# Optimization experiments

Measured on AMD Instinct MI355X. Metric: run time of the kernel, lower is better.

Reference implementation:

```python
import jax, jax.numpy as jnp
import numpy as np
from jax import lax

B, C, H, W = 16, 256, 64, 64
KNUM, KS, STRIDE, PAD, RED, GROUPS = 4, 3, 1, 1, 16, 4
BN_EPS = 1e-5


def setup_inputs() -> dict:
    key = jax.random.key(0)
    ks = jax.random.split(key, 12)
    f = jax.random.normal
    half, red = C // 2, C // RED
    return {
        "x": f(ks[0], (B, C, H, W), jnp.float32),
        "att_conv1d_w": f(ks[1], (3,), jnp.float32) * 0.5,                      # shared Conv1d(1,1,3) in Attention
        "att_out_w": f(ks[2], (C, C), jnp.float32) * (2.0 / C) ** 0.5,          # out_channel_conv2d 1x1
        "att_kernel_w": f(ks[3], (KNUM, C), jnp.float32) * (2.0 / C) ** 0.5,    # kernel_conv2d 1x1
        "ede_weight": f(ks[4], (KNUM, C, C, KS, KS), jnp.float32) * (2.0 / (C * KS * KS)) ** 0.5,
        "lga_conv1d_w": f(ks[5], (3,), jnp.float32) * 0.5,                      # LGA Conv1d(1,1,3) with bias
        "lga_conv1d_b": f(ks[6], (1,), jnp.float32) * 0.1,
        "lga_mlp_w1": f(ks[7], (red, half), jnp.float32) * (2.0 / half) ** 0.5,  # mlp conv 1x1 (no bias)
        "lga_mlp_w2": f(ks[8], (half, red), jnp.float32) * (2.0 / red) ** 0.5,
        "bn_gamma": jnp.ones((C,), jnp.float32),
        "bn_beta": jnp.zeros((C,), jnp.float32),
    }


def _conv1d_same(v_bc, w3):
    # 1-channel cross-correlation along the channel axis, pad=1 (PyTorch Conv1d)
    y = lax.conv_general_dilated(v_bc[:, None, :], w3[None, None, :], (1,), [(1, 1)],
                                 dimension_numbers=("NCH", "OIH", "NCH"))
    return y[:, 0, :]


def reference(x, att_conv1d_w, att_out_w, att_kernel_w, ede_weight,
              lga_conv1d_w, lga_conv1d_b, lga_mlp_w1, lga_mlp_w2,
              bn_gamma, bn_beta):
    b, c, h, w = x.shape

    # ---- EDE (Q branch): dynamic per-sample conv ----
    gap = x.mean(axis=(2, 3))                              # (b, c) global avg pool
    t = _conv1d_same(gap, att_conv1d_w)                    # shared conv1d over channels
    in_att = jax.nn.sigmoid(t)[:, :, None, None]           # (b, c, 1, 1)
    out_att = jax.nn.sigmoid(t @ att_out_w.T)[:, :, None, None]
    k_att = jax.nn.softmax(t @ att_kernel_w.T, axis=1)     # (b, KNUM)
    agg_w = jnp.einsum("bk,koipq->boipq", k_att, ede_weight)  # (b, C, C, KS, KS)
    x_mod = x * in_att

    def per_sample(xi, wi):  # xi: (C,H,W), wi: (C,C,KS,KS)
        return lax.conv_general_dilated(xi[None], wi, (STRIDE, STRIDE),
                                        [(PAD, PAD), (PAD, PAD)])[0]

    Q = jax.vmap(per_sample)(x_mod, agg_w) * out_att       # (b, C, H, W)

    # ---- LGA (K branch) ----
    half = c // 2
    in1, in2 = x[:, :half], x[:, half:]
    s = _conv1d_same(in1.mean(axis=(2, 3)), lga_conv1d_w) + lga_conv1d_b
    x1 = in1 * jax.nn.sigmoid(s)[:, :, None, None]

    def mlp(v):  # (b, half) -> (b, half); 1x1 convs on (b,half,1,1) == matmuls
        return jax.nn.relu(v @ lga_mlp_w1.T) @ lga_mlp_w2.T

    ch = jax.nn.sigmoid(mlp(in2.max(axis=(2, 3))) + mlp(in2.mean(axis=(2, 3))))
    y2 = in2 * ch[:, :, None, None]
    K = jnp.concatenate([x1, y2], axis=1)
    # channel shuffle with GROUPS groups
    K = K.reshape(b, GROUPS, c // GROUPS, h, w).transpose(0, 2, 1, 3, 4).reshape(b, c, h, w)

    # ---- fuse + BatchNorm (training-mode batch stats) + ReLU ----
    z = Q + K
    mean = z.mean(axis=(0, 2, 3))
    var = z.var(axis=(0, 2, 3))
    zn = (z - mean[None, :, None, None]) * lax.rsqrt(var[None, :, None, None] + BN_EPS)
    return jax.nn.relu(zn * bn_gamma[None, :, None, None] + bn_beta[None, :, None, None])
```

## Files before the change

kernel.cpp:

```cpp
#include <hip/hip_runtime.h>
#include <hip/hip_bf16.h>
#include <stdint.h>

#define HW_ 4096

typedef float f32x4 __attribute__((ext_vector_type(4)));
typedef short bf16x8 __attribute__((ext_vector_type(8)));

__device__ __forceinline__ unsigned short f2bf(float f) {
  __hip_bfloat16 h = __float2bfloat16(f);
  return *reinterpret_cast<unsigned short*>(&h);
}
__device__ __forceinline__ float sigmoidf_(float x) { return 1.f / (1.f + __expf(-x)); }

__device__ __forceinline__ void glds16(const void* g, void* l) {
  __builtin_amdgcn_global_load_lds(
      (const __attribute__((address_space(1))) unsigned int*)g,
      (__attribute__((address_space(3))) unsigned int*)l, 16, 0, 0);
}

__global__ void k_pre(const float* __restrict__ x, unsigned short* __restrict__ xtr,
                      float* __restrict__ psum, float* __restrict__ pmax) {
  int hwb = blockIdx.x;
  int cb = blockIdx.y;
  int b = blockIdx.z;
  int t = threadIdx.x;
  __shared__ float sv[64][65];
  int h16 = t & 15, g = t >> 4;
#pragma unroll
  for (int i = 0; i < 4; ++i) {
    int c_l = g + i * 16;
    float4 v = *reinterpret_cast<const float4*>(
        x + (((size_t)b * 256 + cb * 64 + c_l) << 12) + hwb * 64 + h16 * 4);
    *reinterpret_cast<float4*>(&sv[c_l][h16 * 4]) = v;
  }
  __syncthreads();
  {
    int c_l = t >> 2, q = t & 3;
    float s16 = 0.f, m16 = -3.4e38f;
#pragma unroll
    for (int j = 0; j < 16; ++j) {
      float vv = sv[c_l][q * 16 + j];
      s16 += vv; m16 = fmaxf(m16, vv);
    }
    s16 += __shfl_xor(s16, 1); s16 += __shfl_xor(s16, 2);
    m16 = fmaxf(m16, __shfl_xor(m16, 1)); m16 = fmaxf(m16, __shfl_xor(m16, 2));
    if (q == 0) {
      int c = cb * 64 + c_l;
      psum[(((size_t)b * 256 + c) << 6) + hwb] = s16;
      pmax[(((size_t)b * 256 + c) << 6) + hwb] = m16;
    }
  }
#pragma unroll
  for (int i = 0; i < 2; ++i) {
    int fp = t + i * 256;
    int hw2 = fp >> 3;
    int cp = (fp & 7) * 8;
    uint4 uu;
    uu.x = (unsigned)f2bf(sv[cp + 0][hw2]) | ((unsigned)f2bf(sv[cp + 1][hw2]) << 16);
    uu.y = (unsigned)f2bf(sv[cp + 2][hw2]) | ((unsigned)f2bf(sv[cp + 3][hw2]) << 16);
    uu.z = (unsigned)f2bf(sv[cp + 4][hw2]) | ((unsigned)f2bf(sv[cp + 5][hw2]) << 16);
    uu.w = (unsigned)f2bf(sv[cp + 6][hw2]) | ((unsigned)f2bf(sv[cp + 7][hw2]) << 16);
    *reinterpret_cast<uint4*>(xtr + (((size_t)b * 4096 + hwb * 64 + hw2) << 8) + cb * 64 + cp) = uu;
  }
}

__global__ void k_tiny(const float* __restrict__ psum, const float* __restrict__ pmax,
                       const float* __restrict__ aw3, const float* __restrict__ Wout,
                       const float* __restrict__ Wk, const float* __restrict__ lw3,
                       const float* __restrict__ lbia, const float* __restrict__ mw1,
                       const float* __restrict__ mw2,
                       float* __restrict__ in_att, float* __restrict__ out_att,
                       float* __restrict__ katt, float* __restrict__ sc,
                       float* __restrict__ sums, float* __restrict__ zerop) {
  int b = blockIdx.x, t = threadIdx.x;
  __shared__ float g[256], tt[256], red[256], hsum[16], ksm[4], mx[128];
  {
    const float4* pp = reinterpret_cast<const float4*>(psum + ((size_t)(b * 256 + t) << 6));
    const float4* pm = reinterpret_cast<const float4*>(pmax + ((size_t)(b * 256 + t) << 6));
    float s = 0.f, m = -3.4e38f;
#pragma unroll
    for (int j = 0; j < 16; ++j) {
      float4 a = pp[j]; s += (a.x + a.y) + (a.z + a.w);
      float4 q4 = pm[j];
      m = fmaxf(m, fmaxf(fmaxf(q4.x, q4.y), fmaxf(q4.z, q4.w)));
    }
    g[t] = s * (1.f / 4096.f);
    if (t >= 128) mx[t - 128] = m;
  }
  if (b == 0) {
    sums[t] = 0.f; sums[256 + t] = 0.f;
    zerop[t] = 0.f;
  }
  __syncthreads();
  float c0 = aw3[0], c1 = aw3[1], c2 = aw3[2];
  float tv = c1 * g[t];
  if (t > 0) tv += c0 * g[t - 1];
  if (t < 255) tv += c2 * g[t + 1];
  tt[t] = tv;
  in_att[b * 256 + t] = sigmoidf_(tv);
  __syncthreads();
  {
    float d = 0.f;
    const float4* wr = reinterpret_cast<const float4*>(Wout + (size_t)t * 256);
    for (int c4 = 0; c4 < 64; ++c4) {
      float4 wv4 = wr[c4];
      d += tt[c4 * 4] * wv4.x + tt[c4 * 4 + 1] * wv4.y + tt[c4 * 4 + 2] * wv4.z + tt[c4 * 4 + 3] * wv4.w;
    }
    out_att[b * 256 + t] = sigmoidf_(d);
  }
  int k = t >> 6, lane = t & 63;
  {
    float pk = 0.f;
    for (int c = lane; c < 256; c += 64) pk += tt[c] * Wk[k * 256 + c];
    red[t] = pk; __syncthreads();
    for (int off = 32; off > 0; off >>= 1) {
      if (lane < off) red[t] += red[t + off];
      __syncthreads();
    }
    if (t == 0) {
      float l0 = red[0], l1 = red[64], l2 = red[128], l3 = red[192];
      float mm = fmaxf(fmaxf(l0, l1), fmaxf(l2, l3));
      float e0 = __expf(l0 - mm), e1 = __expf(l1 - mm), e2 = __expf(l2 - mm), e3 = __expf(l3 - mm);
      float inv = 1.f / (e0 + e1 + e2 + e3);
      ksm[0] = e0 * inv; ksm[1] = e1 * inv; ksm[2] = e2 * inv; ksm[3] = e3 * inv;
    }
    __syncthreads();
    if (t < 4) katt[b * 4 + t] = ksm[t];
  }
  if (t < 128) {
    float a0 = lw3[0], a1 = lw3[1], a2 = lw3[2];
    float sv = a1 * g[t] + lbia[0];
    if (t > 0) sv += a0 * g[t - 1];
    if (t < 127) sv += a2 * g[t + 1];
    sc[b * 256 + t] = sigmoidf_(sv);
  }
  __syncthreads();
  if (t < 16) {
    float d1 = 0.f, d2 = 0.f;
    const float* w1r = mw1 + t * 128;
    for (int j = 0; j < 128; ++j) { d1 += mx[j] * w1r[j]; d2 += g[128 + j] * w1r[j]; }
    hsum[t] = fmaxf(d1, 0.f) + fmaxf(d2, 0.f);
  }
  __syncthreads();
  if (t < 128) {
    float dd = 0.f;
    const float* w2r = mw2 + t * 16;
    for (int r = 0; r < 16; ++r) dd += hsum[r] * w2r[r];
    sc[b * 256 + 128 + t] = sigmoidf_(dd);
  }
}

__global__ __launch_bounds__(256) void k_agg(const float* __restrict__ ede,
                                             const float* __restrict__ katt,
                                             const float* __restrict__ inatt,
                                             unsigned short* __restrict__ agg) {
  __shared__ float eds[4][2304];
  int o = blockIdx.x, t = threadIdx.x;
#pragma unroll
  for (int k = 0; k < 4; ++k) {
    const float* src = ede + ((size_t)k * 256 + o) * 2304;
#pragma unroll
    for (int j = 0; j < 9; ++j) eds[k][j * 256 + t] = src[j * 256 + t];
  }
  __syncthreads();
  int ii = (t & 127) * 2;
  int bh = t >> 7;
  for (int b2 = 0; b2 < 8; ++b2) {
    int b = b2 * 2 + bh;
    float k0 = katt[b * 4], k1 = katt[b * 4 + 1], k2 = katt[b * 4 + 2], k3 = katt[b * 4 + 3];
    float ia0 = inatt[b * 256 + ii], ia1 = inatt[b * 256 + ii + 1];
    size_t obase = ((size_t)(b * 256 + o) * 9) << 8;
#pragma unroll
    for (int pq = 0; pq < 9; ++pq) {
      float v0 = k0 * eds[0][ii * 9 + pq] + k1 * eds[1][ii * 9 + pq] +
                 k2 * eds[2][ii * 9 + pq] + k3 * eds[3][ii * 9 + pq];
      float v1 = k0 * eds[0][(ii + 1) * 9 + pq] + k1 * eds[1][(ii + 1) * 9 + pq] +
                 k2 * eds[2][(ii + 1) * 9 + pq] + k3 * eds[3][(ii + 1) * 9 + pq];
      v0 *= ia0; v1 *= ia1;
      unsigned int u = (unsigned)f2bf(v0) | ((unsigned)f2bf(v1) << 16);
      *reinterpret_cast<unsigned int*>(agg + obase + (pq << 8) + ii) = u;
    }
  }
}

__global__ __launch_bounds__(512, 2) void k_conv(
    const unsigned short* __restrict__ agg, const unsigned short* __restrict__ xtr,
    const float* __restrict__ x, const float* __restrict__ oatt,
    const float* __restrict__ sc, const float* __restrict__ zerop,
    float* __restrict__ sums, float* __restrict__ zout) {
  __shared__ __align__(16) char smem[147456];
  int wg = blockIdx.x;
  int bswz = ((wg & 7) << 5) | (wg >> 3);
  int b = bswz >> 4, pt = bswz & 15;
  int tid = threadIdx.x;
  int l = tid & 63;
  int wv = tid >> 6;
  int wm = wv >> 2, wn = wv & 3;
  int w0 = l & 15, ks = l >> 4;
  bool maskl0 = (w0 == 0), maskl15 = (w0 == 15);

  int r0 = tid >> 2, s0 = tid & 3;
  int r1 = r0 + 128;
  int f0 = (s0 ^ ((r0 >> 1) & 3)) << 3;
  int f1 = (s0 ^ ((r1 >> 1) & 3)) << 3;
  const unsigned short* aS0 = agg + (size_t)(b * 256 + r0) * 2304 + f0;
  const unsigned short* aS1 = agg + (size_t)(b * 256 + r1) * 2304 + f1;

  auto slabsrc = [&](int j) -> const char* {
    int idx = j * 512 + tid;
    int P = idx >> 2, sp = idx & 3;
    int sr = P >> 6, w = P & 63;
    int imgrow = pt * 4 + sr - 1;
    int ir = imgrow < 0 ? 0 : (imgrow > 63 ? 63 : imgrow);
    int slog = sp ^ ((w >> 1) & 3);
    const char* gp = (const char*)(xtr + (((size_t)b * 4096 + ir * 64 + w) << 8) + slog * 8);
    return ((unsigned)imgrow < 64u) ? gp : (const char*)zerop;
  };
  const char* sb0_ = slabsrc(0);
  const char* sb1_ = slabsrc(1);
  const char* sb2_ = slabsrc(2);

  int aOff[8];
#pragma unroll
  for (int fm = 0; fm < 8; ++fm) {
    int R = wm * 128 + fm * 16 + (l & 15);
    aOff[fm] = R * 64 + (((l >> 4) ^ ((R >> 1) & 3)) << 4);
  }

  f32x4 acc[8][4];
  f32x4 zero4 = {0.f, 0.f, 0.f, 0.f};
#pragma unroll
  for (int i2 = 0; i2 < 8; ++i2)
#pragma unroll
    for (int j2 = 0; j2 < 4; ++j2) acc[i2][j2] = zero4;

  bf16x8 z8 = {0, 0, 0, 0, 0, 0, 0, 0};

  {
    char* sd = smem + 98304;
    glds16(sb0_, sd + tid * 16);
    glds16(sb1_, sd + 8192 + tid * 16);
    glds16(sb2_, sd + 16384 + tid * 16);
    char* ar = smem;
#pragma unroll
    for (int dq = 0; dq < 3; ++dq) {
      glds16(aS0 + dq * 256, ar + dq * 16384 + tid * 16);
      glds16(aS1 + dq * 256, ar + dq * 16384 + 8192 + tid * 16);
    }
  }
  asm volatile("s_waitcnt vmcnt(0)" ::: "memory");
  __builtin_amdgcn_s_barrier();

  int ph = 0;
  for (int c = 0; c < 8; ++c) {
    const char* sb = smem + 98304 + ((c & 1) ? 24576 : 0);
    for (int dp = 0; dp < 3; ++dp, ++ph) {
      if (ph < 23) {
        int nc = (dp == 2) ? c + 1 : c;
        int ndp = (dp == 2) ? 0 : dp + 1;
        char* ar = smem + ((ph + 1) & 1) * 49152;
#pragma unroll
        for (int dq = 0; dq < 3; ++dq) {
          int cols = (ndp * 3 + dq) * 256 + nc * 32;
          glds16(aS0 + cols, ar + dq * 16384 + tid * 16);
          glds16(aS1 + cols, ar + dq * 16384 + 8192 + tid * 16);
        }
      }
      if (dp == 2 && c < 7) {
        char* sd = smem + 98304 + (((c + 1) & 1) ? 24576 : 0);
        glds16(sb0_ + (c + 1) * 64, sd + tid * 16);
        glds16(sb1_ + (c + 1) * 64, sd + 8192 + tid * 16);
        glds16(sb2_ + (c + 1) * 64, sd + 16384 + tid * 16);
      }
      const char* abase = smem + (ph & 1) * 49152;
      int rowb = (wn + dp) << 6;
#pragma unroll
      for (int dq = 0; dq < 3; ++dq) {
        const char* ab = abase + dq * 16384;
        bf16x8 af[8], bv[4];
#pragma unroll
        for (int f = 0; f < 8; ++f) af[f] = *reinterpret_cast<const bf16x8*>(ab + aOff[f]);
#pragma unroll
        for (int fn = 0; fn < 4; ++fn) {
          int wcol = w0 + fn * 16 + (dq - 1);
          int wc = wcol < 0 ? 0 : (wcol > 63 ? 63 : wcol);
          int bo = ((rowb + wc) << 6) + ((ks ^ ((wc >> 1) & 3)) << 4);
          bv[fn] = *reinterpret_cast<const bf16x8*>(sb + bo);
        }
        if (dq == 0) bv[0] = maskl0 ? z8 : bv[0];
        if (dq == 2) bv[3] = maskl15 ? z8 : bv[3];
        __builtin_amdgcn_s_setprio(1);
#pragma unroll
        for (int fm = 0; fm < 8; ++fm)
#pragma unroll
          for (int fn = 0; fn < 4; ++fn)
            acc[fm][fn] = __builtin_amdgcn_mfma_f32_16x16x32_bf16(af[fm], bv[fn], acc[fm][fn], 0, 0, 0);
        __builtin_amdgcn_s_setprio(0);
      }
      asm volatile("s_waitcnt vmcnt(0)" ::: "memory");
      __builtin_amdgcn_s_barrier();
    }
  }
  __syncthreads();

  float* ls = (float*)smem;
  ls[tid] = 0.f;
  __syncthreads();

#pragma unroll
  for (int fm = 0; fm < 8; ++fm) {
#pragma unroll
    for (int r = 0; r < 4; ++r) {
      int m = wm * 128 + fm * 16 + ((l >> 4) << 2) + r;
      int oc = ((m & 3) << 6) | (m >> 2);
      float oav = oatt[b * 256 + m];
      float scv = sc[b * 256 + oc];
      const float* xrow = x + (((size_t)b * 256 + oc) << 12) + pt * 256;
      float* zrow = zout + (((size_t)b * 256 + m) << 12) + pt * 256;
      float psv = 0.f, psv2 = 0.f;
#pragma unroll
      for (int fn = 0; fn < 4; ++fn) {
        int n = wn * 64 + fn * 16 + (l & 15);
        float zv = acc[fm][fn][r] * oav + xrow[n] * scv;
        zrow[n] = zv;
        psv += zv; psv2 += zv * zv;
      }
#pragma unroll
      for (int d = 8; d > 0; d >>= 1) {
        psv += __shfl_down(psv, d, 16);
        psv2 += __shfl_down(psv2, d, 16);
      }
      if ((l & 15) == 0) {
        atomicAdd(&ls[m], psv);
        atomicAdd(&ls[256 + m], psv2);
      }
    }
  }
  __syncthreads();
  if (tid < 256) {
    atomicAdd(&sums[tid], ls[tid]);
    atomicAdd(&sums[256 + tid], ls[256 + tid]);
  }
}

__global__ void k_apply(float* __restrict__ z, const float* __restrict__ sums,
                        const float* __restrict__ gamma, const float* __restrict__ beta) {
  int idx = blockIdx.x * 256 + threadIdx.x;
  for (int i = idx; i < 4194304; i += 4096 * 256) {
    int c = (i >> 10) & 255;
    float mean = sums[c] * (1.f / 65536.f);
    float var = sums[256 + c] * (1.f / 65536.f) - mean * mean;
    float scale = gamma[c] * rsqrtf(var + 1e-5f);
    float shift = beta[c] - mean * scale;
    float4* p = reinterpret_cast<float4*>(z) + i;
    float4 v = *p;
    v.x = fmaxf(v.x * scale + shift, 0.f);
    v.y = fmaxf(v.y * scale + shift, 0.f);
    v.z = fmaxf(v.z * scale + shift, 0.f);
    v.w = fmaxf(v.w * scale + shift, 0.f);
    *p = v;
  }
}

extern "C" void kernel_launch(void* const* d_in, const int* in_sizes, int n_in,
                              void* d_out, int out_size, void* d_ws, size_t ws_size,
                              hipStream_t stream) {
  (void)in_sizes; (void)n_in; (void)out_size; (void)ws_size;
  const float* x = (const float*)d_in[0];
  const float* aw3 = (const float*)d_in[1];
  const float* Wout = (const float*)d_in[2];
  const float* Wk = (const float*)d_in[3];
  const float* ede = (const float*)d_in[4];
  const float* lw3 = (const float*)d_in[5];
  const float* lbia = (const float*)d_in[6];
  const float* mw1 = (const float*)d_in[7];
  const float* mw2 = (const float*)d_in[8];
  const float* gamma = (const float*)d_in[9];
  const float* beta = (const float*)d_in[10];

  char* ws = (char*)d_ws;
  float* inatt = (float*)(ws + 32768);
  float* oatt  = (float*)(ws + 49152);
  float* katt  = (float*)(ws + 65536);
  float* sc    = (float*)(ws + 65792);
  float* zerop = (float*)(ws + 82176);
  float* sums  = (float*)(ws + 83200);
  unsigned short* xtr = (unsigned short*)(ws + 262144);
  unsigned short* agg = (unsigned short*)(ws + 262144 + 33554432);
  float* psum = (float*)(ws + 262144 + 33554432);
  float* pmax = (float*)(ws + 262144 + 33554432 + 1048576);
  float* z = (float*)d_out;

  k_pre<<<dim3(64, 4, 16), 256, 0, stream>>>(x, xtr, psum, pmax);
  k_tiny<<<16, 256, 0, stream>>>(psum, pmax, aw3, Wout, Wk, lw3, lbia, mw1, mw2,
                                 inatt, oatt, katt, sc, sums, zerop);
  k_agg<<<256, 256, 0, stream>>>(ede, katt, inatt, agg);
  k_conv<<<256, 512, 0, stream>>>(agg, xtr, x, oatt, sc, zerop, sums, z);
  k_apply<<<4096, 256, 0, stream>>>(z, sums, gamma, beta);
}
```

Before: 148.9 us.

## Load conv weights directly from global in MFMA fragment layout, bypassing LDS

The aggregation kernel now writes the per-sample dynamic weights in an order that matches the MFMA A-fragment layout. The conv kernel then loads A fragments straight from global memory into registers, prefetching one tap ahead. This removes the LDS staging of the weights and most per-tap barriers, and shrinks shared memory from 144KB to 48KB, which may allow more workgroups per CU. In exchange, global load latency now sits directly in the MFMA loop, each wave re-reads weights with no sharing across waves, and the double-buffered fragments raise register pressure.

```diff
diff --git a/kernel.cpp b/kernel.cpp
--- a/kernel.cpp
+++ b/kernel.cpp
@@ -166,11 +166,12 @@
   __syncthreads();
   int ii = (t & 127) * 2;
   int bh = t >> 7;
+  int fg = o >> 4, r = o & 15;
+  int cs = ii >> 5, lh = (ii >> 3) & 3, jj = ii & 7;
   for (int b2 = 0; b2 < 8; ++b2) {
     int b = b2 * 2 + bh;
     float k0 = katt[b * 4], k1 = katt[b * 4 + 1], k2 = katt[b * 4 + 2], k3 = katt[b * 4 + 3];
     float ia0 = inatt[b * 256 + ii], ia1 = inatt[b * 256 + ii + 1];
-    size_t obase = ((size_t)(b * 256 + o) * 9) << 8;
 #pragma unroll
     for (int pq = 0; pq < 9; ++pq) {
       float v0 = k0 * eds[0][ii * 9 + pq] + k1 * eds[1][ii * 9 + pq] +
@@ -179,7 +180,8 @@
                  k2 * eds[2][(ii + 1) * 9 + pq] + k3 * eds[3][(ii + 1) * 9 + pq];
       v0 *= ia0; v1 *= ia1;
       unsigned int u = (unsigned)f2bf(v0) | ((unsigned)f2bf(v1) << 16);
-      *reinterpret_cast<unsigned int*>(agg + obase + (pq << 8) + ii) = u;
+      size_t base = (((((size_t)(b * 9 + pq) * 8 + cs) * 16 + fg) * 64 + lh * 16 + r) << 3) + jj;
+      *reinterpret_cast<unsigned int*>(agg + base) = u;
     }
   }
 }
@@ -189,7 +191,7 @@
     const float* __restrict__ x, const float* __restrict__ oatt,
     const float* __restrict__ sc, const float* __restrict__ zerop,
     float* __restrict__ sums, float* __restrict__ zout) {
-  __shared__ __align__(16) char smem[147456];
+  __shared__ __align__(16) char smem[49152];
   int wg = blockIdx.x;
   int bswz = ((wg & 7) << 5) | (wg >> 3);
   int b = bswz >> 4, pt = bswz & 15;
@@ -199,13 +201,6 @@
   int wm = wv >> 2, wn = wv & 3;
   int w0 = l & 15, ks = l >> 4;
   bool maskl0 = (w0 == 0), maskl15 = (w0 == 15);
-
-  int r0 = tid >> 2, s0 = tid & 3;
-  int r1 = r0 + 128;
-  int f0 = (s0 ^ ((r0 >> 1) & 3)) << 3;
-  int f1 = (s0 ^ ((r1 >> 1) & 3)) << 3;
-  const unsigned short* aS0 = agg + (size_t)(b * 256 + r0) * 2304 + f0;
-  const unsigned short* aS1 = agg + (size_t)(b * 256 + r1) * 2304 + f1;
 
   auto slabsrc = [&](int j) -> const char* {
     int idx = j * 512 + tid;
@@ -221,12 +216,9 @@
   const char* sb1_ = slabsrc(1);
   const char* sb2_ = slabsrc(2);
 
-  int aOff[8];
-#pragma unroll
-  for (int fm = 0; fm < 8; ++fm) {
-    int R = wm * 128 + fm * 16 + (l & 15);
-    aOff[fm] = R * 64 + (((l >> 4) ^ ((R >> 1) & 3)) << 4);
-  }
+  auto aP = [&](int pq, int cs, int fm) -> const unsigned short* {
+    return agg + (((((size_t)(b * 9 + pq) * 8 + cs) * 16 + wm * 8 + fm) << 9)) + l * 8;
+  };
 
   f32x4 acc[8][4];
   f32x4 zero4 = {0.f, 0.f, 0.f, 0.f};
@@ -236,71 +228,61 @@
     for (int j2 = 0; j2 < 4; ++j2) acc[i2][j2] = zero4;
 
   bf16x8 z8 = {0, 0, 0, 0, 0, 0, 0, 0};
-
-  {
-    char* sd = smem + 98304;
+  bf16x8 af[8], afn[8];
+
+  {
+    char* sd = smem;
     glds16(sb0_, sd + tid * 16);
     glds16(sb1_, sd + 8192 + tid * 16);
     glds16(sb2_, sd + 16384 + tid * 16);
-    char* ar = smem;
-#pragma unroll
-    for (int dq = 0; dq < 3; ++dq) {
-      glds16(aS0 + dq * 256, ar + dq * 16384 + tid * 16);
-      glds16(aS1 + dq * 256, ar + dq * 16384 + 8192 + tid * 16);
-    }
-  }
+  }
+#pragma unroll
+  for (int fm = 0; fm < 8; ++fm) af[fm] = *reinterpret_cast<const bf16x8*>(aP(0, 0, fm));
   asm volatile("s_waitcnt vmcnt(0)" ::: "memory");
   __builtin_amdgcn_s_barrier();
 
-  int ph = 0;
   for (int c = 0; c < 8; ++c) {
-    const char* sb = smem + 98304 + ((c & 1) ? 24576 : 0);
-    for (int dp = 0; dp < 3; ++dp, ++ph) {
-      if (ph < 23) {
-        int nc = (dp == 2) ? c + 1 : c;
-        int ndp = (dp == 2) ? 0 : dp + 1;
-        char* ar = smem + ((ph + 1) & 1) * 49152;
-#pragma unroll
-        for (int dq = 0; dq < 3; ++dq) {
-          int cols = (ndp * 3 + dq) * 256 + nc * 32;
-          glds16(aS0 + cols, ar + dq * 16384 + tid * 16);
-          glds16(aS1 + cols, ar + dq * 16384 + 8192 + tid * 16);
-        }
-      }
-      if (dp == 2 && c < 7) {
-        char* sd = smem + 98304 + (((c + 1) & 1) ? 24576 : 0);
-        glds16(sb0_ + (c + 1) * 64, sd + tid * 16);
-        glds16(sb1_ + (c + 1) * 64, sd + 8192 + tid * 16);
-        glds16(sb2_ + (c + 1) * 64, sd + 16384 + tid * 16);
-      }
-      const char* abase = smem + (ph & 1) * 49152;
+    const char* sb = smem + ((c & 1) ? 24576 : 0);
+    if (c < 7) {
+      char* sd = smem + (((c + 1) & 1) ? 24576 : 0);
+      glds16(sb0_ + (c + 1) * 64, sd + tid * 16);
+      glds16(sb1_ + (c + 1) * 64, sd + 8192 + tid * 16);
+      glds16(sb2_ + (c + 1) * 64, sd + 16384 + tid * 16);
+    }
+    int cn = (c < 7) ? c + 1 : 7;
+#pragma unroll
+    for (int pq = 0; pq < 9; ++pq) {
+      const int dp = pq / 3, dq = pq % 3;
+      {
+        const int npq = (pq < 8) ? pq + 1 : 0;
+        int ncs = (pq < 8) ? c : cn;
+#pragma unroll
+        for (int fm = 0; fm < 8; ++fm)
+          afn[fm] = *reinterpret_cast<const bf16x8*>(aP(npq, ncs, fm));
+      }
+      bf16x8 bv[4];
       int rowb = (wn + dp) << 6;
 #pragma unroll
-      for (int dq = 0; dq < 3; ++dq) {
-        const char* ab = abase + dq * 16384;
-        bf16x8 af[8], bv[4];
-#pragma unroll
-        for (int f = 0; f < 8; ++f) af[f] = *reinterpret_cast<const bf16x8*>(ab + aOff[f]);
-#pragma unroll
-        for (int fn = 0; fn < 4; ++fn) {
-          int wcol = w0 + fn * 16 + (dq - 1);
-          int wc = wcol < 0 ? 0 : (wcol > 63 ? 63 : wcol);
-          int bo = ((rowb + wc) << 6) + ((ks ^ ((wc >> 1) & 3)) << 4);
-          bv[fn] = *reinterpret_cast<const bf16x8*>(sb + bo);
-        }
-        if (dq == 0) bv[0] = maskl0 ? z8 : bv[0];
-        if (dq == 2) bv[3] = maskl15 ? z8 : bv[3];
-        __builtin_amdgcn_s_setprio(1);
-#pragma unroll
-        for (int fm = 0; fm < 8; ++fm)
-#pragma unroll
-          for (int fn = 0; fn < 4; ++fn)
-            acc[fm][fn] = __builtin_amdgcn_mfma_f32_16x16x32_bf16(af[fm], bv[fn], acc[fm][fn], 0, 0, 0);
-        __builtin_amdgcn_s_setprio(0);
-      }
-      asm volatile("s_waitcnt vmcnt(0)" ::: "memory");
-      __builtin_amdgcn_s_barrier();
-    }
+      for (int fn = 0; fn < 4; ++fn) {
+        int wcol = w0 + fn * 16 + (dq - 1);
+        int wc = wcol < 0 ? 0 : (wcol > 63 ? 63 : wcol);
+        int bo = ((rowb + wc) << 6) + ((ks ^ ((wc >> 1) & 3)) << 4);
+        bv[fn] = *reinterpret_cast<const bf16x8*>(sb + bo);
+      }
+      if (dq == 0) bv[0] = maskl0 ? z8 : bv[0];
+      if (dq == 2) bv[3] = maskl15 ? z8 : bv[3];
+      __builtin_amdgcn_s_setprio(1);
+#pragma unroll
+      for (int fm = 0; fm < 8; ++fm)
+#pragma unroll
+        for (int fn = 0; fn < 4; ++fn)
+          acc[fm][fn] = __builtin_amdgcn_mfma_f32_16x16x32_bf16(af[fm], bv[fn], acc[fm][fn], 0, 0, 0);
+      __builtin_amdgcn_s_setprio(0);
+#pragma unroll
+      for (int fm = 0; fm < 8; ++fm) af[fm] = afn[fm];
+    }
+    asm volatile("s_waitcnt vmcnt(0)" ::: "memory");
+    __builtin_amdgcn_s_barrier();
   }
   __syncthreads();
 
```

Result: slower. 161.0 us (+8.1%).
